# Kernel optimization log

Measured on AMD Instinct MI355X. Metric: run time of the kernel, lower is better.

Reference implementation:

```python
import jax, jax.numpy as jnp
import numpy as np

C, C1, C2 = 64, 8, 32  # channels, channels//8, channels//2
B, H, W = 4, 64, 64


def conv1x1(x, w, b):
    # x: [B,C_in,H,W], w: [C_out,C_in], b: [C_out]
    return jnp.einsum('bchw,oc->bohw', x, w) + b[None, :, None, None]


def setup_inputs() -> dict:
    key = jax.random.key(0)
    ks = jax.random.split(key, 9)
    s_in = 1.0 / np.sqrt(C)
    s_c2 = 1.0 / np.sqrt(C2)
    return {
        'nonlocal_input': jax.random.normal(ks[0], (B, C, H, W), jnp.float32),
        'Wd': jax.random.uniform(ks[1], (C1, C), jnp.float32, -s_in, s_in),
        'bd': jax.random.uniform(ks[2], (C1,), jnp.float32, -s_in, s_in),
        'Wp': jax.random.uniform(ks[3], (C1, C), jnp.float32, -s_in, s_in),
        'bp': jax.random.uniform(ks[4], (C1,), jnp.float32, -s_in, s_in),
        'Wg': jax.random.uniform(ks[5], (C2, C), jnp.float32, -s_in, s_in),
        'bg': jax.random.uniform(ks[6], (C2,), jnp.float32, -s_in, s_in),
        'Wl': jax.random.uniform(ks[7], (C, C2), jnp.float32, -s_c2, s_c2),
        'bl': jax.random.uniform(ks[8], (C,), jnp.float32, -s_c2, s_c2),
    }


def reference(nonlocal_input, Wd, bd, Wp, bp, Wg, bg, Wl, bl):
    x = nonlocal_input
    b, c, h, w = x.shape
    hw = h * w

    # delta: [B,C1,H,W] -> permute(0,2,3,1) -> [B,HW,C1]
    delta = conv1x1(x, Wd, bd).transpose(0, 2, 3, 1).reshape(b, hw, C1)

    # phi: [B,C1,H,W] -> permute(1,0,2,3) -> [C1,B,H,W] -> reshape [B,C1,HW]
    # (faithful to the original, which mixes batch/channel axes here)
    phi = conv1x1(x, Wp, bp).transpose(1, 0, 2, 3).reshape(b, C1, hw)

    scores = jnp.einsum('bnc,bcm->bnm', delta, phi)  # [B,HW,HW]
    # softmax over the fully-flattened [HW*HW] axis per batch element
    attn = jax.nn.softmax(scores.reshape(b, hw * hw), axis=1).reshape(b, hw, hw)

    g = conv1x1(x, Wg, bg).transpose(0, 2, 3, 1).reshape(b, hw, C2)  # [B,HW,C2]
    out = jnp.einsum('bnm,bmc->bnc', attn, g)  # [B,HW,C2]
    out = out.reshape(b, h, w, C2).transpose(0, 3, 1, 2)  # [B,C2,H,W]
    return x + conv1x1(out, Wl, bl)
```

## Files before the change

kernel.cpp:

```cpp
#include <hip/hip_runtime.h>
#include <math.h>

#define HW   4096
#define CIN  64
#define NC1  8
#define NC2  32
#define NB   4
#define MS   4

typedef __attribute__((ext_vector_type(8))) short short8;
typedef __attribute__((ext_vector_type(4))) float f32x4;

#define OFF_DBF   0u
#define OFF_PBF   65536u
#define OFF_GT    131072u
#define OFF_ACC   393216u
#define ACC_STRIDE 524288u
#define OFF_ZPART 2490368u

__device__ __forceinline__ ushort f2bf(float f) {
    unsigned u = __float_as_uint(f);
    return (ushort)((u + 0x8000u) >> 16);
}

__global__ __launch_bounds__(256) void k_proj(
    const float* __restrict__ x,
    const float* __restrict__ Wd, const float* __restrict__ bd,
    const float* __restrict__ Wp, const float* __restrict__ bp,
    const float* __restrict__ Wg, const float* __restrict__ bg,
    ushort* __restrict__ dbf, ushort* __restrict__ pbf, ushort* __restrict__ gt)
{
    int gid = blockIdx.x * 256 + threadIdx.x;
    int grp = gid >> 14;
    int pf  = gid & 16383;
    int b   = pf >> 12;
    int pos = pf & 4095;

    const float* xb = x + (size_t)b * CIN * HW + pos;

    float a[12];
    if (grp == 0) {
        #pragma unroll
        for (int k = 0; k < 8; ++k) a[k] = bd[k];
        #pragma unroll
        for (int k = 0; k < 4; ++k) a[8 + k] = bp[k];
        #pragma unroll
        for (int c = 0; c < CIN; ++c) {
            float v = xb[(size_t)c * HW];
            #pragma unroll
            for (int k = 0; k < 8; ++k) a[k] = fmaf(v, Wd[k * CIN + c], a[k]);
            #pragma unroll
            for (int k = 0; k < 4; ++k) a[8 + k] = fmaf(v, Wp[k * CIN + c], a[8 + k]);
        }
        short8 dv;
        #pragma unroll
        for (int k = 0; k < 8; ++k) dv[k] = (short)f2bf(a[k]);
        *(short8*)(dbf + (size_t)(b * HW + pos) * NC1) = dv;
        #pragma unroll
        for (int k = 0; k < 4; ++k) {
            int r = k * NB + b; int i = r >> 3; int j = r & 7;
            pbf[((size_t)i * HW + pos) * NC1 + j] = f2bf(a[8 + k]);
        }
    } else if (grp == 1) {
        #pragma unroll
        for (int k = 0; k < 4; ++k) a[k] = bp[4 + k];
        #pragma unroll
        for (int k = 0; k < 8; ++k) a[4 + k] = bg[k];
        #pragma unroll
        for (int c = 0; c < CIN; ++c) {
            float v = xb[(size_t)c * HW];
            #pragma unroll
            for (int k = 0; k < 4; ++k) a[k] = fmaf(v, Wp[(4 + k) * CIN + c], a[k]);
            #pragma unroll
            for (int k = 0; k < 8; ++k) a[4 + k] = fmaf(v, Wg[k * CIN + c], a[4 + k]);
        }
        #pragma unroll
        for (int k = 0; k < 4; ++k) {
            int r = (4 + k) * NB + b; int i = r >> 3; int j = r & 7;
            pbf[((size_t)i * HW + pos) * NC1 + j] = f2bf(a[k]);
        }
        #pragma unroll
        for (int k = 0; k < 8; ++k)
            gt[((size_t)b * NC2 + k) * HW + pos] = f2bf(a[4 + k]);
    } else if (grp == 2) {
        #pragma unroll
        for (int k = 0; k < 12; ++k) a[k] = bg[8 + k];
        #pragma unroll
        for (int c = 0; c < CIN; ++c) {
            float v = xb[(size_t)c * HW];
            #pragma unroll
            for (int k = 0; k < 12; ++k) a[k] = fmaf(v, Wg[(8 + k) * CIN + c], a[k]);
        }
        #pragma unroll
        for (int k = 0; k < 12; ++k)
            gt[((size_t)b * NC2 + 8 + k) * HW + pos] = f2bf(a[k]);
    } else {
        #pragma unroll
        for (int k = 0; k < 12; ++k) a[k] = bg[20 + k];
        #pragma unroll
        for (int c = 0; c < CIN; ++c) {
            float v = xb[(size_t)c * HW];
            #pragma unroll
            for (int k = 0; k < 12; ++k) a[k] = fmaf(v, Wg[(20 + k) * CIN + c], a[k]);
        }
        #pragma unroll
        for (int k = 0; k < 12; ++k)
            gt[((size_t)b * NC2 + 20 + k) * HW + pos] = f2bf(a[k]);
    }
}

__global__ __launch_bounds__(256, 2) void k_attn(
    const ushort* __restrict__ dbf, const ushort* __restrict__ pbf,
    const ushort* __restrict__ gt, float* __restrict__ acc_out,
    float* __restrict__ zpart)
{
    __shared__ __align__(16) ushort plds[4][16 * 40];
    __shared__ float zred[4];

    int bid = blockIdx.x;
    int b   = bid >> 8;
    int nt  = (bid >> 2) & 63;
    int ms  = bid & 3;
    int tid = threadIdx.x;
    int w   = tid >> 6;
    int l   = tid & 63;
    int l15 = l & 15;
    int g   = l >> 4;
    int n0  = nt * 64 + w * 16;
    int mb0 = ms * 1024;

    const short8 zero8 = {0, 0, 0, 0, 0, 0, 0, 0};
    const f32x4  zero4 = {0.f, 0.f, 0.f, 0.f};

    short8 adelta = zero8;
    if (g == 0)
        adelta = *(const short8*)(dbf + (size_t)(b * HW + n0 + l15) * NC1);

    f32x4 acc0 = zero4, acc1 = zero4;
    float z = 0.f;
    ushort* myP = &plds[w][0];

    const ushort* pb = pbf + (size_t)b * HW * NC1;
    const ushort* gb = gt  + (size_t)b * NC2 * HW;

    for (int mc = 0; mc < 32; ++mc) {
        int mb = mb0 + mc * 32;

        short8 bg0 = *(const short8*)(gb + (size_t)l15 * HW + mb + g * 8);
        short8 bg1 = *(const short8*)(gb + (size_t)(l15 + 16) * HW + mb + g * 8);

        short8 bphi0 = zero8, bphi1 = zero8;
        if (g == 0) {
            bphi0 = *(const short8*)(pb + (size_t)(mb + l15) * NC1);
            bphi1 = *(const short8*)(pb + (size_t)(mb + 16 + l15) * NC1);
        }

        f32x4 s0 = __builtin_amdgcn_mfma_f32_16x16x32_bf16(adelta, bphi0, zero4, 0, 0, 0);
        f32x4 s1 = __builtin_amdgcn_mfma_f32_16x16x32_bf16(adelta, bphi1, zero4, 0, 0, 0);

        #pragma unroll
        for (int r = 0; r < 4; ++r) {
            float e0 = __expf(s0[r]);
            float e1 = __expf(s1[r]);
            z += e0 + e1;
            int row = 4 * g + r;
            myP[row * 40 + l15]      = f2bf(e0);
            myP[row * 40 + 16 + l15] = f2bf(e1);
        }

        short8 pa = *(const short8*)(myP + l15 * 40 + g * 8);
        acc0 = __builtin_amdgcn_mfma_f32_16x16x32_bf16(pa, bg0, acc0, 0, 0, 0);
        acc1 = __builtin_amdgcn_mfma_f32_16x16x32_bf16(pa, bg1, acc1, 0, 0, 0);
    }

    float* ao = acc_out + (size_t)ms * ACC_STRIDE + ((size_t)b * HW + n0) * NC2;
    #pragma unroll
    for (int r = 0; r < 4; ++r) {
        int row = 4 * g + r;
        ao[(size_t)row * NC2 + l15]      = acc0[r];
        ao[(size_t)row * NC2 + 16 + l15] = acc1[r];
    }

    #pragma unroll
    for (int off = 32; off > 0; off >>= 1) z += __shfl_xor(z, off);
    if (l == 0) zred[w] = z;
    __syncthreads();
    if (tid == 0) zpart[bid] = zred[0] + zred[1] + zred[2] + zred[3];
}

__global__ __launch_bounds__(256) void k_conv(
    const float* __restrict__ x, const float* __restrict__ Wl,
    const float* __restrict__ bl, const float* __restrict__ acc,
    const float* __restrict__ zpart, float* __restrict__ out)
{
    int gid = blockIdx.x * 256 + threadIdx.x;
    int grp = gid >> 14;
    int pf  = gid & 16383;
    int b   = pf >> 12;
    int pos = pf & 4095;

    float Z = 0.f;
    const float4* zp = (const float4*)(zpart + b * 256);
    #pragma unroll
    for (int i = 0; i < 64; ++i) {
        float4 v = zp[i];
        Z += v.x + v.y + v.z + v.w;
    }
    float inv = 1.0f / Z;

    float on_[NC2];
    #pragma unroll
    for (int j = 0; j < NC2; ++j) on_[j] = 0.f;
    #pragma unroll
    for (int s = 0; s < MS; ++s) {
        const float4* ap = (const float4*)(acc + (size_t)s * ACC_STRIDE +
                                           ((size_t)b * HW + pos) * NC2);
        #pragma unroll
        for (int q = 0; q < 8; ++q) {
            float4 v = ap[q];
            on_[q * 4 + 0] += v.x; on_[q * 4 + 1] += v.y;
            on_[q * 4 + 2] += v.z; on_[q * 4 + 3] += v.w;
        }
    }
    #pragma unroll
    for (int j = 0; j < NC2; ++j) on_[j] *= inv;

    const float* xb = x + (size_t)b * CIN * HW + pos;
    float* ob = out + (size_t)b * CIN * HW + pos;
    #pragma unroll
    for (int oo = 0; oo < 16; ++oo) {
        int o = grp * 16 + oo;
        float r = xb[(size_t)o * HW] + bl[o];
        #pragma unroll
        for (int j = 0; j < NC2; ++j) r = fmaf(Wl[o * NC2 + j], on_[j], r);
        ob[(size_t)o * HW] = r;
    }
}

extern "C" void kernel_launch(void* const* d_in, const int* in_sizes, int n_in,
                              void* d_out, int out_size, void* d_ws, size_t ws_size,
                              hipStream_t stream) {
    const float* x  = (const float*)d_in[0];
    const float* Wd = (const float*)d_in[1];
    const float* bd = (const float*)d_in[2];
    const float* Wp = (const float*)d_in[3];
    const float* bp = (const float*)d_in[4];
    const float* Wg = (const float*)d_in[5];
    const float* bg = (const float*)d_in[6];
    const float* Wl = (const float*)d_in[7];
    const float* bl = (const float*)d_in[8];
    float* ws = (float*)d_ws;

    ushort* dbf = (ushort*)(ws + OFF_DBF);
    ushort* pbf = (ushort*)(ws + OFF_PBF);
    ushort* gt  = (ushort*)(ws + OFF_GT);

    k_proj<<<256, 256, 0, stream>>>(x, Wd, bd, Wp, bp, Wg, bg, dbf, pbf, gt);
    k_attn<<<1024, 256, 0, stream>>>(dbf, pbf, gt, ws + OFF_ACC, ws + OFF_ZPART);
    k_conv<<<256, 256, 0, stream>>>(x, Wl, bl, ws + OFF_ACC, ws + OFF_ZPART,
                                    (float*)d_out);
}
```

Before: 133.5 us.

## Replace LDS transpose of attention probabilities with register permlane swaps; split M 8-way

```diff
diff --git a/kernel.cpp b/kernel.cpp
--- a/kernel.cpp
+++ b/kernel.cpp
@@ -6,17 +6,17 @@
 #define NC1  8
 #define NC2  32
 #define NB   4
-#define MS   4
+#define MS   8
 
 typedef __attribute__((ext_vector_type(8))) short short8;
 typedef __attribute__((ext_vector_type(4))) float f32x4;
 
-#define OFF_DBF   0u
-#define OFF_PBF   65536u
-#define OFF_GT    131072u
-#define OFF_ACC   393216u
+#define OFF_DBF    0u
+#define OFF_PBF    65536u
+#define OFF_GT     131072u
+#define OFF_ACC    393216u
 #define ACC_STRIDE 524288u
-#define OFF_ZPART 2490368u
+#define OFF_ZPART  4587520u
 
 __device__ __forceinline__ ushort f2bf(float f) {
     unsigned u = __float_as_uint(f);
@@ -109,68 +109,83 @@
     }
 }
 
-__global__ __launch_bounds__(256, 2) void k_attn(
+__global__ __launch_bounds__(256, 4) void k_attn(
     const ushort* __restrict__ dbf, const ushort* __restrict__ pbf,
     const ushort* __restrict__ gt, float* __restrict__ acc_out,
     float* __restrict__ zpart)
 {
-    __shared__ __align__(16) ushort plds[4][16 * 40];
     __shared__ float zred[4];
 
     int bid = blockIdx.x;
-    int b   = bid >> 8;
-    int nt  = (bid >> 2) & 63;
-    int ms  = bid & 3;
+    int b   = bid >> 9;
+    int rem = bid & 511;
+    int nt  = rem >> 3;
+    int ms  = rem & 7;
     int tid = threadIdx.x;
     int w   = tid >> 6;
     int l   = tid & 63;
     int l15 = l & 15;
     int g   = l >> 4;
     int n0  = nt * 64 + w * 16;
-    int mb0 = ms * 1024;
+    int mb0 = ms * 512;
+    bool godd = (g & 1) != 0;
 
     const short8 zero8 = {0, 0, 0, 0, 0, 0, 0, 0};
     const f32x4  zero4 = {0.f, 0.f, 0.f, 0.f};
 
-    short8 adelta = zero8;
+    short8 bdelta = zero8;
     if (g == 0)
-        adelta = *(const short8*)(dbf + (size_t)(b * HW + n0 + l15) * NC1);
+        bdelta = *(const short8*)(dbf + (size_t)(b * HW + n0 + l15) * NC1);
 
     f32x4 acc0 = zero4, acc1 = zero4;
     float z = 0.f;
-    ushort* myP = &plds[w][0];
 
     const ushort* pb = pbf + (size_t)b * HW * NC1;
     const ushort* gb = gt  + (size_t)b * NC2 * HW;
 
-    for (int mc = 0; mc < 32; ++mc) {
+    for (int mc = 0; mc < 16; ++mc) {
         int mb = mb0 + mc * 32;
 
         short8 bg0 = *(const short8*)(gb + (size_t)l15 * HW + mb + g * 8);
         short8 bg1 = *(const short8*)(gb + (size_t)(l15 + 16) * HW + mb + g * 8);
 
-        short8 bphi0 = zero8, bphi1 = zero8;
+        short8 aphi0 = zero8, aphi1 = zero8;
         if (g == 0) {
-            bphi0 = *(const short8*)(pb + (size_t)(mb + l15) * NC1);
-            bphi1 = *(const short8*)(pb + (size_t)(mb + 16 + l15) * NC1);
-        }
-
-        f32x4 s0 = __builtin_amdgcn_mfma_f32_16x16x32_bf16(adelta, bphi0, zero4, 0, 0, 0);
-        f32x4 s1 = __builtin_amdgcn_mfma_f32_16x16x32_bf16(adelta, bphi1, zero4, 0, 0, 0);
-
-        #pragma unroll
-        for (int r = 0; r < 4; ++r) {
-            float e0 = __expf(s0[r]);
-            float e1 = __expf(s1[r]);
-            z += e0 + e1;
-            int row = 4 * g + r;
-            myP[row * 40 + l15]      = f2bf(e0);
-            myP[row * 40 + 16 + l15] = f2bf(e1);
-        }
-
-        short8 pa = *(const short8*)(myP + l15 * 40 + g * 8);
-        acc0 = __builtin_amdgcn_mfma_f32_16x16x32_bf16(pa, bg0, acc0, 0, 0, 0);
-        acc1 = __builtin_amdgcn_mfma_f32_16x16x32_bf16(pa, bg1, acc1, 0, 0, 0);
+            aphi0 = *(const short8*)(pb + (size_t)(mb + l15) * NC1);
+            aphi1 = *(const short8*)(pb + (size_t)(mb + 16 + l15) * NC1);
+        }
+
+        f32x4 s0 = __builtin_amdgcn_mfma_f32_16x16x32_bf16(aphi0, bdelta, zero4, 0, 0, 0);
+        f32x4 s1 = __builtin_amdgcn_mfma_f32_16x16x32_bf16(aphi1, bdelta, zero4, 0, 0, 0);
+
+        float e0 = __expf(s0[0]), e1 = __expf(s0[1]);
+        float e2 = __expf(s0[2]), e3 = __expf(s0[3]);
+        float e4 = __expf(s1[0]), e5 = __expf(s1[1]);
+        float e6 = __expf(s1[2]), e7 = __expf(s1[3]);
+        z += ((e0 + e1) + (e2 + e3)) + ((e4 + e5) + (e6 + e7));
+
+        int A0, A1, B0v, B1v;
+        asm("v_cvt_pk_bf16_f32 %0, %1, %2" : "=v"(A0)  : "v"(e0), "v"(e1));
+        asm("v_cvt_pk_bf16_f32 %0, %1, %2" : "=v"(A1)  : "v"(e2), "v"(e3));
+        asm("v_cvt_pk_bf16_f32 %0, %1, %2" : "=v"(B0v) : "v"(e4), "v"(e5));
+        asm("v_cvt_pk_bf16_f32 %0, %1, %2" : "=v"(B1v) : "v"(e6), "v"(e7));
+
+        asm("v_permlane32_swap_b32 %0, %1" : "+v"(A0), "+v"(B0v));
+        asm("v_permlane32_swap_b32 %0, %1" : "+v"(A1), "+v"(B1v));
+
+        int X0  = __shfl_xor(A0, 16);
+        int X1  = __shfl_xor(A1, 16);
+        int Xq0 = __shfl_xor(B0v, 16);
+        int Xq1 = __shfl_xor(B1v, 16);
+
+        union { int u[4]; short8 s8; } pa;
+        pa.u[0] = godd ? Xq0 : A0;
+        pa.u[1] = godd ? Xq1 : A1;
+        pa.u[2] = godd ? B0v : X0;
+        pa.u[3] = godd ? B1v : X1;
+
+        acc0 = __builtin_amdgcn_mfma_f32_16x16x32_bf16(pa.s8, bg0, acc0, 0, 0, 0);
+        acc1 = __builtin_amdgcn_mfma_f32_16x16x32_bf16(pa.s8, bg1, acc1, 0, 0, 0);
     }
 
     float* ao = acc_out + (size_t)ms * ACC_STRIDE + ((size_t)b * HW + n0) * NC2;
@@ -193,20 +208,21 @@
     const float* __restrict__ bl, const float* __restrict__ acc,
     const float* __restrict__ zpart, float* __restrict__ out)
 {
+    __shared__ float zl[4];
+
     int gid = blockIdx.x * 256 + threadIdx.x;
     int grp = gid >> 14;
     int pf  = gid & 16383;
     int b   = pf >> 12;
     int pos = pf & 4095;
-
-    float Z = 0.f;
-    const float4* zp = (const float4*)(zpart + b * 256);
-    #pragma unroll
-    for (int i = 0; i < 64; ++i) {
-        float4 v = zp[i];
-        Z += v.x + v.y + v.z + v.w;
-    }
-    float inv = 1.0f / Z;
+    int tid = threadIdx.x;
+
+    float zv = zpart[b * 512 + tid] + zpart[b * 512 + 256 + tid];
+    #pragma unroll
+    for (int off = 32; off > 0; off >>= 1) zv += __shfl_xor(zv, off);
+    if ((tid & 63) == 0) zl[tid >> 6] = zv;
+    __syncthreads();
+    float inv = 1.0f / (zl[0] + zl[1] + zl[2] + zl[3]);
 
     float on_[NC2];
     #pragma unroll
@@ -256,7 +272,7 @@
     ushort* gt  = (ushort*)(ws + OFF_GT);
 
     k_proj<<<256, 256, 0, stream>>>(x, Wd, bd, Wp, bp, Wg, bg, dbf, pbf, gt);
-    k_attn<<<1024, 256, 0, stream>>>(dbf, pbf, gt, ws + OFF_ACC, ws + OFF_ZPART);
+    k_attn<<<2048, 256, 0, stream>>>(dbf, pbf, gt, ws + OFF_ACC, ws + OFF_ZPART);
     k_conv<<<256, 256, 0, stream>>>(x, Wl, bl, ws + OFF_ACC, ws + OFF_ZPART,
                                     (float*)d_out);
 }
```

New measurement: 144.6 us. +8.3%, slower.
